# Kernel optimization log

Measured on AMD Instinct MI355X. Metric: run time of the kernel, lower is better.

## Reference

```python
import jax, jax.numpy as jnp
import numpy as np

B, C, H, W = 2, 256, 64, 64
NUM_HEADS = 4
DIM_HEAD_QK = 64
DIM_HEAD_V = 64  # dim_out // num_heads
DIM_OUT_QK = NUM_HEADS * DIM_HEAD_QK  # 256
DIM_OUT_V = NUM_HEADS * DIM_HEAD_V    # 256
SCALE = DIM_HEAD_QK ** -0.5


def rel_logits_1d(q, rel_k, permute):
    # q: (Bh, Hq, Wq, d), rel_k: (2*Wq-1, d)
    Bh, Hq, Wq, d = q.shape
    R = 2 * Wq - 1
    x = jnp.einsum('bhwd,rd->bhwr', q, rel_k)              # (Bh, Hq, Wq, R)
    x = x.reshape(-1, Wq, R)
    x_pad = jnp.pad(x, ((0, 0), (0, 0), (0, 1))).reshape(x.shape[0], -1)
    x_pad = jnp.pad(x_pad, ((0, 0), (0, Wq - 1)))
    x_pad = x_pad.reshape(-1, Wq + 1, R)
    x = x_pad[:, :Wq, Wq - 1:]                              # (Bh*Hq, Wq, Wq)
    x = x.reshape(Bh, Hq, 1, Wq, Wq)
    x = jnp.broadcast_to(x, (Bh, Hq, Hq, Wq, Wq))
    return jnp.transpose(x, permute)


def pos_embed_rel(q, height_rel, width_rel):
    # q: (Bh, HW, d)
    Bh = q.shape[0]
    qr = q.reshape(Bh, H, W, -1)
    rel_w = rel_logits_1d(qr, width_rel, (0, 1, 3, 2, 4))   # (Bh, H, W, H, W)
    qt = jnp.transpose(qr, (0, 2, 1, 3))                    # (Bh, W, H, d)
    rel_h = rel_logits_1d(qt, height_rel, (0, 3, 1, 4, 2))  # (Bh, H, W, H, W)
    return (rel_h + rel_w).reshape(Bh, H * W, H * W)


def setup_inputs() -> dict:
    key = jax.random.key(0)
    k1, k2, k3, k4 = jax.random.split(key, 4)
    x = jax.random.normal(k1, (B, C, H, W), dtype=jnp.float32)
    qkv_w = jax.random.normal(k2, (2 * DIM_OUT_QK + DIM_OUT_V, C), dtype=jnp.float32) * (C ** -0.5)
    height_rel = jax.random.normal(k3, (2 * H - 1, DIM_HEAD_QK), dtype=jnp.float32) * SCALE
    width_rel = jax.random.normal(k4, (2 * W - 1, DIM_HEAD_QK), dtype=jnp.float32) * SCALE
    return {"x": x, "qkv_w": qkv_w, "height_rel": height_rel, "width_rel": width_rel}


def reference(x, qkv_w, height_rel, width_rel):
    # 1x1 conv == channel matmul
    qkv = jnp.einsum('bchw,oc->bohw', x, qkv_w)             # (B, 768, H, W)
    q, k, v = jnp.split(qkv, [DIM_OUT_QK, 2 * DIM_OUT_QK], axis=1)
    HW = H * W
    q = q.reshape(B * NUM_HEADS, DIM_HEAD_QK, HW).transpose(0, 2, 1)  # (Bh, HW, d)
    k = k.reshape(B * NUM_HEADS, DIM_HEAD_QK, HW)                     # (Bh, d, HW)
    v = v.reshape(B * NUM_HEADS, DIM_HEAD_V, HW).transpose(0, 2, 1)   # (Bh, HW, dv)
    attn = jnp.einsum('bnd,bdm->bnm', q, k) * SCALE + pos_embed_rel(q, height_rel, width_rel)
    attn = jax.nn.softmax(attn, axis=-1)
    out = jnp.einsum('bnm,bmd->bnd', attn, v)               # (Bh, HW, dv)
    out = out.transpose(0, 2, 1).reshape(B, DIM_OUT_V, H, W)
    return out
```

## Files before the change

kernel.cpp:

```cpp
#include <hip/hip_runtime.h>
#include <hip/hip_bf16.h>

typedef __attribute__((ext_vector_type(8))) short bf16x8;
typedef __attribute__((ext_vector_type(4))) float f32x4;

static __device__ __forceinline__ f32x4 mfma16(bf16x8 a, bf16x8 b, f32x4 c) {
    return __builtin_amdgcn_mfma_f32_16x16x32_bf16(a, b, c, 0, 0, 0);
}
static __device__ __forceinline__ void gll16(const void* g, void* l) {
    __builtin_amdgcn_global_load_lds(
        (const __attribute__((address_space(1))) unsigned int*)g,
        (__attribute__((address_space(3))) unsigned int*)l, 16, 0, 0);
}

#define LOG2E 1.44269504f

__global__ __launch_bounds__(256, 4) void qkv_kernel(
    const float* __restrict__ x, const float* __restrict__ w,
    __hip_bfloat16* __restrict__ qb, __hip_bfloat16* __restrict__ kb,
    __hip_bfloat16* __restrict__ vt)
{
    alignas(16) __shared__ __hip_bfloat16 sA[64 * 72];
    alignas(16) __shared__ __hip_bfloat16 sB[64 * 72];
    const int nb = blockIdx.x * 64;
    const int ob = blockIdx.y * 64;
    const int b  = blockIdx.z;
    const int tid  = threadIdx.x;
    const int lane = tid & 63;
    const int wv   = tid >> 6;
    const int quad = lane >> 4;
    const int l16  = lane & 15;

    f32x4 acc[4];
    for (int i = 0; i < 4; i++) acc[i] = (f32x4)0.f;

    const int oA = tid >> 2, cA = (tid & 3) << 4;
    const float* srcw = w + (ob + oA) * 256 + cA;
    const int cB = tid >> 2, nB = (tid & 3) << 4;
    const int csw = cB ^ ((tid & 3) * 16);
    const float* srcx = x + ((size_t)b * 256 + cB) * 4096 + nb + nB;

    float4 ra[4], rb4[4];
    #pragma unroll
    for (int i = 0; i < 4; i++) ra[i]  = *(const float4*)(srcw + i * 4);
    #pragma unroll
    for (int i = 0; i < 4; i++) rb4[i] = *(const float4*)(srcx + i * 4);

    for (int t = 0; t < 4; t++) {
        __syncthreads();
        {
            union { bf16x8 v; __hip_bfloat16 h[8]; } u0, u1;
            #pragma unroll
            for (int i = 0; i < 2; i++) {
                float4 f = ra[i];
                u0.h[4*i+0] = __float2bfloat16(f.x); u0.h[4*i+1] = __float2bfloat16(f.y);
                u0.h[4*i+2] = __float2bfloat16(f.z); u0.h[4*i+3] = __float2bfloat16(f.w);
            }
            #pragma unroll
            for (int i = 0; i < 2; i++) {
                float4 f = ra[2 + i];
                u1.h[4*i+0] = __float2bfloat16(f.x); u1.h[4*i+1] = __float2bfloat16(f.y);
                u1.h[4*i+2] = __float2bfloat16(f.z); u1.h[4*i+3] = __float2bfloat16(f.w);
            }
            *(bf16x8*)&sA[oA * 72 + cA]     = u0.v;
            *(bf16x8*)&sA[oA * 72 + cA + 8] = u1.v;
        }
        {
            #pragma unroll
            for (int i = 0; i < 4; i++) {
                float4 f = rb4[i];
                sB[(nB + 4*i + 0) * 72 + csw] = __float2bfloat16(f.x);
                sB[(nB + 4*i + 1) * 72 + csw] = __float2bfloat16(f.y);
                sB[(nB + 4*i + 2) * 72 + csw] = __float2bfloat16(f.z);
                sB[(nB + 4*i + 3) * 72 + csw] = __float2bfloat16(f.w);
            }
        }
        __syncthreads();
        if (t < 3) {
            #pragma unroll
            for (int i = 0; i < 4; i++)
                ra[i]  = *(const float4*)(srcw + (t + 1) * 64 + i * 4);
            #pragma unroll
            for (int i = 0; i < 4; i++)
                rb4[i] = *(const float4*)(srcx + (size_t)(t + 1) * 64 * 4096 + i * 4);
        }
        const __hip_bfloat16* aRow = &sA[(16 * wv + l16) * 72];
        #pragma unroll
        for (int ks = 0; ks < 2; ks++) {
            bf16x8 af = *(const bf16x8*)&aRow[ks * 32 + quad * 8];
            #pragma unroll
            for (int ct = 0; ct < 4; ct++) {
                bf16x8 bfv = *(const bf16x8*)&sB[(16 * ct + l16) * 72
                                                 + ((ks * 32 + quad * 8) ^ (ct * 16))];
                acc[ct] = mfma16(af, bfv, acc[ct]);
            }
        }
    }
    if (ob < 512) {
        __syncthreads();
        #pragma unroll
        for (int ct = 0; ct < 4; ct++) {
            union { short4 s; __hip_bfloat16 hh[4]; } u;
            #pragma unroll
            for (int r = 0; r < 4; r++) u.hh[r] = __float2bfloat16(acc[ct][r]);
            *(short4*)&sA[(16 * ct + l16) * 72 + 16 * wv + 4 * quad] = u.s;
        }
        __syncthreads();
        const int n_l = tid >> 2, d16 = (tid & 3) * 16;
        const int n = nb + n_l;
        const __hip_bfloat16* srcl = &sA[n_l * 72 + d16];
        bf16x8 v0 = *(const bf16x8*)srcl;
        bf16x8 v1 = *(const bf16x8*)(srcl + 8);
        const int bhh = b * 4 + ((ob & 255) >> 6);
        if (ob < 256) {
            __hip_bfloat16* dst = qb + ((size_t)bhh * 4096 + n) * 64;
            *(bf16x8*)(dst + d16)     = v0;
            *(bf16x8*)(dst + d16 + 8) = v1;
        } else {
            const int s = (n & 7) << 3;
            __hip_bfloat16* dst = kb + ((size_t)bhh * 4096 + n) * 64;
            *(bf16x8*)(dst + (d16 ^ s))       = v0;
            *(bf16x8*)(dst + ((d16 + 8) ^ s)) = v1;
        }
    } else {
        __syncthreads();
        #pragma unroll
        for (int ct = 0; ct < 4; ct++)
            #pragma unroll
            for (int r = 0; r < 4; r++)
                sA[(16 * wv + quad * 4 + r) * 72 + 16 * ct + l16] = __float2bfloat16(acc[ct][r]);
        int o2 = (ob - 512) + 16 * wv + l16;
        int bhh = b * 4 + (o2 >> 6), d = o2 & 63;
        const __hip_bfloat16* srcl = &sA[(16 * wv + l16) * 72 + 16 * quad];
        __hip_bfloat16* vrow = vt + ((size_t)bhh * 64 + d) * 4096;
        const int kt = quad & 1;
        const int gbase = nb + (quad >> 1) * 32;
        const int dsw = (d & 7) << 3;
        #pragma unroll
        for (int m = 0; m < 4; m++) {
            short4 val = *(const short4*)(srcl + 4 * m);
            int P4 = gbase + 8 * m + 4 * kt;
            *(short4*)(vrow + (P4 ^ dsw)) = val;
        }
    }
}

__global__ __launch_bounds__(512, 4) void attn_kernel(
    const __hip_bfloat16* __restrict__ qb, const __hip_bfloat16* __restrict__ kb,
    const __hip_bfloat16* __restrict__ vt, const float* __restrict__ hrel,
    const float* __restrict__ wrel, float* __restrict__ out)
{
    extern __shared__ __align__(16) char smem[];
    alignas(16) __shared__ __hip_bfloat16 sRH[64 * 66];

    const int h    = blockIdx.x;
    const int bh   = blockIdx.y;
    const int tid  = threadIdx.x;
    const int lane = tid & 63;
    const int wv   = tid >> 6;
    const int qg   = wv >> 2;
    const int kg   = wv & 3;
    const int quad = lane >> 4;
    const int l16  = lane & 15;

    __hip_bfloat16* sQ   = (__hip_bfloat16*)smem;
    __hip_bfloat16* sW   = (__hip_bfloat16*)smem + 64 * 72;
    __hip_bfloat16* sHRs = (__hip_bfloat16*)smem + 192 * 72;
    __hip_bfloat16* sRWt = (__hip_bfloat16*)smem;

    {
        int r = tid >> 3, d8 = (tid & 7) * 8;
        *(bf16x8*)&sQ[r * 72 + d8] =
            *(const bf16x8*)&qb[(((size_t)bh * 4096 + h * 64 + r)) * 64 + d8];
    }
    {
        int r = tid >> 2, c0 = (tid & 3) << 4;
        union { bf16x8 v; __hip_bfloat16 h8[8]; } u0, u1;
        #pragma unroll
        for (int i = 0; i < 2; i++) {
            float4 f = (r < 127) ? *(const float4*)&wrel[r * 64 + c0 + 4*i] : float4{0,0,0,0};
            u0.h8[4*i+0] = __float2bfloat16(f.x); u0.h8[4*i+1] = __float2bfloat16(f.y);
            u0.h8[4*i+2] = __float2bfloat16(f.z); u0.h8[4*i+3] = __float2bfloat16(f.w);
        }
        #pragma unroll
        for (int i = 0; i < 2; i++) {
            float4 f = (r < 127) ? *(const float4*)&wrel[r * 64 + c0 + 8 + 4*i] : float4{0,0,0,0};
            u1.h8[4*i+0] = __float2bfloat16(f.x); u1.h8[4*i+1] = __float2bfloat16(f.y);
            u1.h8[4*i+2] = __float2bfloat16(f.z); u1.h8[4*i+3] = __float2bfloat16(f.w);
        }
        *(bf16x8*)&sW[r * 72 + c0]     = u0.v;
        *(bf16x8*)&sW[r * 72 + c0 + 8] = u1.v;
    }
    {
        int r = tid >> 3, c0 = (tid & 7) * 8;
        union { bf16x8 v; __hip_bfloat16 h8[8]; } u0;
        #pragma unroll
        for (int i = 0; i < 2; i++) {
            float4 f = *(const float4*)&hrel[(63 - h + r) * 64 + c0 + 4*i];
            u0.h8[4*i+0] = __float2bfloat16(f.x); u0.h8[4*i+1] = __float2bfloat16(f.y);
            u0.h8[4*i+2] = __float2bfloat16(f.z); u0.h8[4*i+3] = __float2bfloat16(f.w);
        }
        *(bf16x8*)&sHRs[r * 72 + c0] = u0.v;
    }
    __syncthreads();

    const int g    = wv & 3;
    const int half = wv >> 2;
    const __hip_bfloat16* aRow = &sQ[(16 * g + l16) * 72];
    bf16x8 qf0 = *(const bf16x8*)&aRow[quad * 8];
    bf16x8 qf1 = *(const bf16x8*)&aRow[32 + quad * 8];
    bf16x8 qm[2][2];
    #pragma unroll
    for (int qt = 0; qt < 2; qt++) {
        const __hip_bfloat16* qr = &sQ[(qg * 32 + 16 * qt + l16) * 72];
        qm[qt][0] = *(const bf16x8*)&qr[quad * 8];
        qm[qt][1] = *(const bf16x8*)&qr[32 + quad * 8];
    }
    __syncthreads();

    {
        const int rbase = half * 64;
        #pragma unroll
        for (int ct = 0; ct < 4; ct++) {
            int rr = rbase + 16 * ct + l16;
            f32x4 a = (f32x4)0.f;
            a = mfma16(qf0, *(const bf16x8*)&sW[rr * 72 + quad * 8], a);
            a = mfma16(qf1, *(const bf16x8*)&sW[rr * 72 + 32 + quad * 8], a);
            #pragma unroll
            for (int r = 0; r < 4; r++) {
                int ww = 16 * g + quad * 4 + r;
                int wp = rr + ww - 63;
                if (wp >= 0 && wp < 64) sRWt[ww * 68 + wp] = __float2bfloat16(a[r]);
            }
        }
    }
    if (half == 0) {
        #pragma unroll
        for (int ct = 0; ct < 4; ct++) {
            f32x4 a = (f32x4)0.f;
            a = mfma16(qf0, *(const bf16x8*)&sHRs[(16 * ct + l16) * 72 + quad * 8], a);
            a = mfma16(qf1, *(const bf16x8*)&sHRs[(16 * ct + l16) * 72 + 32 + quad * 8], a);
            #pragma unroll
            for (int r = 0; r < 4; r++)
                sRH[(16 * g + quad * 4 + r) * 66 + 16 * ct + l16] = __float2bfloat16(a[r]);
        }
    }
    __syncthreads();

    union S4 { short4 s; __hip_bfloat16 h[4]; };
    float rwf[2][2][4];
    #pragma unroll
    for (int qt = 0; qt < 2; qt++)
        #pragma unroll
        for (int kt = 0; kt < 2; kt++) {
            S4 t;
            t.s = *(const short4*)&sRWt[(qg * 32 + 16 * qt + l16) * 68
                                        + 32 * (kg & 1) + 16 * kt + 4 * quad];
            #pragma unroll
            for (int r = 0; r < 4; r++)
                rwf[qt][kt][r] = LOG2E * __bfloat162float(t.h[r]);
        }
    __syncthreads();

    const char* kT = (const char*)kb + (size_t)bh * 524288 + wv * 1024 + lane * 16;
    const char* vT = (const char*)vt + (size_t)bh * 524288
                     + (size_t)(wv * 4 + quad) * 8192 + l16 * 16;

    gll16(kT,                smem + wv * 1024);
    gll16(kT + 8192,         smem + 8192 + wv * 1024);
    gll16(vT,                smem + 16384 + wv * 1024);
    gll16(vT + 262144,       smem + 24576 + wv * 1024);
    gll16(kT + 16384,        smem + 32768 + wv * 1024);
    gll16(kT + 16384 + 8192, smem + 32768 + 8192 + wv * 1024);
    gll16(vT + 256,          smem + 32768 + 16384 + wv * 1024);
    gll16(vT + 262144 + 256, smem + 32768 + 24576 + wv * 1024);

    f32x4 oacc[2][4];
    #pragma unroll
    for (int qt = 0; qt < 2; qt++)
        #pragma unroll
        for (int dt = 0; dt < 4; dt++) oacc[qt][dt] = (f32x4)0.f;
    f32x4 lacc[2] = {(f32x4)0.f, (f32x4)0.f};
    const bf16x8 vones = (bf16x8)(short)0x3F80;

    const int krowOff = (kg * 32 + l16) * 128;
    const int sw  = (l16 & 7) << 4;
    const int kA  = (quad * 16) ^ sw;
    const int kB  = (64 + quad * 16) ^ sw;
    const int vOff = 16384 + l16 * 256 + ((kg * 64 + quad * 16) ^ sw);

    const __hip_bfloat16* rh0 = &sRH[(qg * 32 + l16) * 66];
    const __hip_bfloat16* rh1 = &sRH[(qg * 32 + 16 + l16) * 66];
    const float SC = 0.125f * LOG2E;

    for (int j = 0; j < 32; j++) {
        const char* buf = smem + (j & 1) * 32768;
        if (j < 31) asm volatile("s_waitcnt vmcnt(4)" ::: "memory");
        else        asm volatile("s_waitcnt vmcnt(0)" ::: "memory");
        __builtin_amdgcn_s_barrier();
        __builtin_amdgcn_sched_barrier(0);

        const char* kr = buf + krowOff;
        bf16x8 kf00 = *(const bf16x8*)(kr + kA);
        bf16x8 kf01 = *(const bf16x8*)(kr + kB);
        bf16x8 kf10 = *(const bf16x8*)(kr + 2048 + kA);
        bf16x8 kf11 = *(const bf16x8*)(kr + 2048 + kB);

        f32x4 s[2][2];
        __builtin_amdgcn_s_setprio(1);
        #pragma unroll
        for (int qt = 0; qt < 2; qt++) {
            f32x4 a0 = (f32x4)0.f, a1 = (f32x4)0.f;
            a0 = mfma16(kf00, qm[qt][0], a0);
            a0 = mfma16(kf01, qm[qt][1], a0);
            a1 = mfma16(kf10, qm[qt][0], a1);
            a1 = mfma16(kf11, qm[qt][1], a1);
            s[qt][0] = a0; s[qt][1] = a1;
        }
        __builtin_amdgcn_s_setprio(0);

        const int hp = 2 * j + (kg >> 1);
        bf16x8 pa[2];
        #pragma unroll
        for (int qt = 0; qt < 2; qt++) {
            float rhb = LOG2E * __bfloat162float((qt ? rh1 : rh0)[hp]);
            float pv[8];
            #pragma unroll
            for (int r = 0; r < 4; r++)
                pv[r] = __builtin_amdgcn_exp2f(fmaf(s[qt][0][r], SC, rwf[qt][0][r] + rhb));
            #pragma unroll
            for (int r = 0; r < 4; r++)
                pv[4 + r] = __builtin_amdgcn_exp2f(fmaf(s[qt][1][r], SC, rwf[qt][1][r] + rhb));
            union { bf16x8 v; __hip_bfloat162 b2[4]; } pu;
            #pragma unroll
            for (int pi = 0; pi < 4; pi++)
                pu.b2[pi] = __float22bfloat162_rn(float2{pv[2 * pi], pv[2 * pi + 1]});
            pa[qt] = pu.v;
        }

        __builtin_amdgcn_s_setprio(1);
        #pragma unroll
        for (int dt = 0; dt < 4; dt++) {
            bf16x8 vf = *(const bf16x8*)(buf + vOff + dt * 4096);
            oacc[0][dt] = mfma16(pa[0], vf, oacc[0][dt]);
            oacc[1][dt] = mfma16(pa[1], vf, oacc[1][dt]);
        }
        lacc[0] = mfma16(pa[0], vones, lacc[0]);
        lacc[1] = mfma16(pa[1], vones, lacc[1]);
        __builtin_amdgcn_s_setprio(0);

        __builtin_amdgcn_sched_barrier(0);
        __builtin_amdgcn_s_barrier();
        if (j < 30) {
            char* nb2 = smem + (j & 1) * 32768;
            const char* gk = kT + (size_t)(j + 2) * 16384;
            gll16(gk,          nb2 + wv * 1024);
            gll16(gk + 8192,   nb2 + 8192 + wv * 1024);
            const char* gv = vT + (size_t)(j + 2) * 256;
            gll16(gv,          nb2 + 16384 + wv * 1024);
            gll16(gv + 262144, nb2 + 24576 + wv * 1024);
        }
    }

    float* obuf = (float*)smem;
    if (kg != 0) {
        float* rb = obuf + (kg - 1) * 4672;
        #pragma unroll
        for (int qt = 0; qt < 2; qt++)
            #pragma unroll
            for (int dt = 0; dt < 4; dt++)
                *(f32x4*)&rb[qg * 2304 + (16 * dt + l16) * 36 + 16 * qt + 4 * quad]
                    = oacc[qt][dt];
        if (l16 == 0)
            #pragma unroll
            for (int qt = 0; qt < 2; qt++)
                #pragma unroll
                for (int r = 0; r < 4; r++)
                    rb[4608 + qg * 32 + 16 * qt + 4 * quad + r] = lacc[qt][r];
    }
    __syncthreads();
    if (kg == 0) {
        #pragma unroll
        for (int rg = 0; rg < 3; rg++) {
            const float* rb = obuf + rg * 4672;
            #pragma unroll
            for (int qt = 0; qt < 2; qt++) {
                #pragma unroll
                for (int dt = 0; dt < 4; dt++)
                    oacc[qt][dt] += *(const f32x4*)&rb[qg * 2304 + (16 * dt + l16) * 36
                                                       + 16 * qt + 4 * quad];
                #pragma unroll
                for (int r = 0; r < 4; r++)
                    lacc[qt][r] += rb[4608 + qg * 32 + 16 * qt + 4 * quad + r];
            }
        }
        const int b = bh >> 2, head = bh & 3;
        #pragma unroll
        for (int qt = 0; qt < 2; qt++) {
            f32x4 lv;
            #pragma unroll
            for (int r = 0; r < 4; r++) lv[r] = 1.f / lacc[qt][r];
            #pragma unroll
            for (int dt = 0; dt < 4; dt++) {
                f32x4 o = oacc[qt][dt] * lv;
                int dv = 16 * dt + l16;
                int q0 = qg * 32 + 16 * qt + 4 * quad;
                *(f32x4*)&out[((size_t)(b * 256 + head * 64 + dv)) * 4096 + h * 64 + q0] = o;
            }
        }
    }
}

extern "C" void kernel_launch(void* const* d_in, const int* in_sizes, int n_in,
                              void* d_out, int out_size, void* d_ws, size_t ws_size,
                              hipStream_t stream) {
    const float* x     = (const float*)d_in[0];
    const float* qkv_w = (const float*)d_in[1];
    const float* hrel  = (const float*)d_in[2];
    const float* wrel  = (const float*)d_in[3];
    float* out = (float*)d_out;

    __hip_bfloat16* qb = (__hip_bfloat16*)d_ws;
    __hip_bfloat16* kb = qb + (size_t)8 * 4096 * 64;
    __hip_bfloat16* vt = kb + (size_t)8 * 4096 * 64;

    qkv_kernel<<<dim3(64, 12, 2), 256, 0, stream>>>(x, qkv_w, qb, kb, vt);
    attn_kernel<<<dim3(64, 8), 512, 65536, stream>>>(qb, kb, vt, hrel, wrel, out);
}
```

Baseline: 127.8 us.

## Replace LDS double-buffered K/V staging with direct global register loads

Drops the global_load_lds double-buffering of K and V tiles through shared memory, along with the per-iteration barriers and vmcnt waits. Each wave now loads its K and V fragments straight from global memory (L2) into registers, prefetching the next K tile one step ahead with a ping-pong register pair. The rel-width bias is kept as packed bf16 and converted inside the loop instead of being held as floats. This removes LDS traffic and block-wide synchronisation, but adds redundant global loads across waves, exposes V-load latency within each step, and raises register pressure.

```diff
diff --git a/kernel.cpp b/kernel.cpp
--- a/kernel.cpp
+++ b/kernel.cpp
@@ -6,11 +6,6 @@
 
 static __device__ __forceinline__ f32x4 mfma16(bf16x8 a, bf16x8 b, f32x4 c) {
     return __builtin_amdgcn_mfma_f32_16x16x32_bf16(a, b, c, 0, 0, 0);
-}
-static __device__ __forceinline__ void gll16(const void* g, void* l) {
-    __builtin_amdgcn_global_load_lds(
-        (const __attribute__((address_space(1))) unsigned int*)g,
-        (__attribute__((address_space(3))) unsigned int*)l, 16, 0, 0);
 }
 
 #define LOG2E 1.44269504f
@@ -248,32 +243,14 @@
     __syncthreads();
 
     union S4 { short4 s; __hip_bfloat16 h[4]; };
-    float rwf[2][2][4];
+    S4 rwp[2][2];
     #pragma unroll
     for (int qt = 0; qt < 2; qt++)
         #pragma unroll
-        for (int kt = 0; kt < 2; kt++) {
-            S4 t;
-            t.s = *(const short4*)&sRWt[(qg * 32 + 16 * qt + l16) * 68
-                                        + 32 * (kg & 1) + 16 * kt + 4 * quad];
-            #pragma unroll
-            for (int r = 0; r < 4; r++)
-                rwf[qt][kt][r] = LOG2E * __bfloat162float(t.h[r]);
-        }
+        for (int kt = 0; kt < 2; kt++)
+            rwp[qt][kt].s = *(const short4*)&sRWt[(qg * 32 + 16 * qt + l16) * 68
+                                                  + 32 * (kg & 1) + 16 * kt + 4 * quad];
     __syncthreads();
-
-    const char* kT = (const char*)kb + (size_t)bh * 524288 + wv * 1024 + lane * 16;
-    const char* vT = (const char*)vt + (size_t)bh * 524288
-                     + (size_t)(wv * 4 + quad) * 8192 + l16 * 16;
-
-    gll16(kT,                smem + wv * 1024);
-    gll16(kT + 8192,         smem + 8192 + wv * 1024);
-    gll16(vT,                smem + 16384 + wv * 1024);
-    gll16(vT + 262144,       smem + 24576 + wv * 1024);
-    gll16(kT + 16384,        smem + 32768 + wv * 1024);
-    gll16(kT + 16384 + 8192, smem + 32768 + 8192 + wv * 1024);
-    gll16(vT + 256,          smem + 32768 + 16384 + wv * 1024);
-    gll16(vT + 262144 + 256, smem + 32768 + 24576 + wv * 1024);
 
     f32x4 oacc[2][4];
     #pragma unroll
@@ -283,84 +260,101 @@
     f32x4 lacc[2] = {(f32x4)0.f, (f32x4)0.f};
     const bf16x8 vones = (bf16x8)(short)0x3F80;
 
-    const int krowOff = (kg * 32 + l16) * 128;
     const int sw  = (l16 & 7) << 4;
-    const int kA  = (quad * 16) ^ sw;
-    const int kB  = (64 + quad * 16) ^ sw;
-    const int vOff = 16384 + l16 * 256 + ((kg * 64 + quad * 16) ^ sw);
+    const int ko0 = (quad * 16) ^ sw;
+    const int ko1 = (64 + quad * 16) ^ sw;
+    const char* kgb = (const char*)kb + (size_t)bh * 524288 + (kg * 32 + l16) * 128;
+    const char* vgb = (const char*)vt + (size_t)bh * 524288 + (size_t)l16 * 8192
+                      + ((kg * 64 + quad * 16) ^ sw);
 
     const __hip_bfloat16* rh0 = &sRH[(qg * 32 + l16) * 66];
     const __hip_bfloat16* rh1 = &sRH[(qg * 32 + 16 + l16) * 66];
     const float SC = 0.125f * LOG2E;
 
-    for (int j = 0; j < 32; j++) {
-        const char* buf = smem + (j & 1) * 32768;
-        if (j < 31) asm volatile("s_waitcnt vmcnt(4)" ::: "memory");
-        else        asm volatile("s_waitcnt vmcnt(0)" ::: "memory");
-        __builtin_amdgcn_s_barrier();
-        __builtin_amdgcn_sched_barrier(0);
-
-        const char* kr = buf + krowOff;
-        bf16x8 kf00 = *(const bf16x8*)(kr + kA);
-        bf16x8 kf01 = *(const bf16x8*)(kr + kB);
-        bf16x8 kf10 = *(const bf16x8*)(kr + 2048 + kA);
-        bf16x8 kf11 = *(const bf16x8*)(kr + 2048 + kB);
-
-        f32x4 s[2][2];
-        __builtin_amdgcn_s_setprio(1);
-        #pragma unroll
-        for (int qt = 0; qt < 2; qt++) {
-            f32x4 a0 = (f32x4)0.f, a1 = (f32x4)0.f;
-            a0 = mfma16(kf00, qm[qt][0], a0);
-            a0 = mfma16(kf01, qm[qt][1], a0);
-            a1 = mfma16(kf10, qm[qt][0], a1);
-            a1 = mfma16(kf11, qm[qt][1], a1);
-            s[qt][0] = a0; s[qt][1] = a1;
-        }
-        __builtin_amdgcn_s_setprio(0);
-
-        const int hp = 2 * j + (kg >> 1);
-        bf16x8 pa[2];
-        #pragma unroll
-        for (int qt = 0; qt < 2; qt++) {
-            float rhb = LOG2E * __bfloat162float((qt ? rh1 : rh0)[hp]);
-            float pv[8];
-            #pragma unroll
-            for (int r = 0; r < 4; r++)
-                pv[r] = __builtin_amdgcn_exp2f(fmaf(s[qt][0][r], SC, rwf[qt][0][r] + rhb));
-            #pragma unroll
-            for (int r = 0; r < 4; r++)
-                pv[4 + r] = __builtin_amdgcn_exp2f(fmaf(s[qt][1][r], SC, rwf[qt][1][r] + rhb));
-            union { bf16x8 v; __hip_bfloat162 b2[4]; } pu;
-            #pragma unroll
-            for (int pi = 0; pi < 4; pi++)
-                pu.b2[pi] = __float22bfloat162_rn(float2{pv[2 * pi], pv[2 * pi + 1]});
-            pa[qt] = pu.v;
-        }
-
-        __builtin_amdgcn_s_setprio(1);
-        #pragma unroll
-        for (int dt = 0; dt < 4; dt++) {
-            bf16x8 vf = *(const bf16x8*)(buf + vOff + dt * 4096);
-            oacc[0][dt] = mfma16(pa[0], vf, oacc[0][dt]);
-            oacc[1][dt] = mfma16(pa[1], vf, oacc[1][dt]);
-        }
-        lacc[0] = mfma16(pa[0], vones, lacc[0]);
-        lacc[1] = mfma16(pa[1], vones, lacc[1]);
-        __builtin_amdgcn_s_setprio(0);
-
-        __builtin_amdgcn_sched_barrier(0);
-        __builtin_amdgcn_s_barrier();
-        if (j < 30) {
-            char* nb2 = smem + (j & 1) * 32768;
-            const char* gk = kT + (size_t)(j + 2) * 16384;
-            gll16(gk,          nb2 + wv * 1024);
-            gll16(gk + 8192,   nb2 + 8192 + wv * 1024);
-            const char* gv = vT + (size_t)(j + 2) * 256;
-            gll16(gv,          nb2 + 16384 + wv * 1024);
-            gll16(gv + 262144, nb2 + 24576 + wv * 1024);
-        }
-    }
+#define LOAD_K(D, jj) do {                                        \
+        const char* kp_ = kgb + (size_t)(jj) * 16384;             \
+        D##0 = *(const bf16x8*)(kp_ + ko0);                       \
+        D##1 = *(const bf16x8*)(kp_ + ko1);                       \
+        D##2 = *(const bf16x8*)(kp_ + 2048 + ko0);                \
+        D##3 = *(const bf16x8*)(kp_ + 2048 + ko1);                \
+    } while (0)
+
+#define STEP(jj, KC, KN, doPref) do {                                          \
+        const char* vp_ = vgb + (size_t)(jj) * 256;                            \
+        bf16x8 vv0 = *(const bf16x8*)(vp_);                                    \
+        bf16x8 vv1 = *(const bf16x8*)(vp_ + 131072);                           \
+        bf16x8 vv2 = *(const bf16x8*)(vp_ + 262144);                           \
+        bf16x8 vv3 = *(const bf16x8*)(vp_ + 393216);                           \
+        if (doPref) LOAD_K(KN, (jj) + 1);                                      \
+        f32x4 s00, s01, s10, s11;                                              \
+        __builtin_amdgcn_s_setprio(1);                                         \
+        s00 = mfma16(KC##0, qm[0][0], (f32x4)0.f);                             \
+        s00 = mfma16(KC##1, qm[0][1], s00);                                    \
+        s10 = mfma16(KC##2, qm[0][0], (f32x4)0.f);                             \
+        s10 = mfma16(KC##3, qm[0][1], s10);                                    \
+        s01 = mfma16(KC##0, qm[1][0], (f32x4)0.f);                             \
+        s01 = mfma16(KC##1, qm[1][1], s01);                                    \
+        s11 = mfma16(KC##2, qm[1][0], (f32x4)0.f);                             \
+        s11 = mfma16(KC##3, qm[1][1], s11);                                    \
+        __builtin_amdgcn_s_setprio(0);                                         \
+        const int hp_ = 2 * (jj) + (kg >> 1);                                  \
+        float rhb0 = LOG2E * __bfloat162float(rh0[hp_]);                       \
+        float rhb1 = LOG2E * __bfloat162float(rh1[hp_]);                       \
+        bf16x8 pa0, pa1;                                                       \
+        {                                                                      \
+            float pvv[8];                                                      \
+            _Pragma("unroll")                                                  \
+            for (int r = 0; r < 4; r++)                                        \
+                pvv[r] = __builtin_amdgcn_exp2f(fmaf(s00[r], SC,               \
+                    fmaf(__bfloat162float(rwp[0][0].h[r]), LOG2E, rhb0)));     \
+            _Pragma("unroll")                                                  \
+            for (int r = 0; r < 4; r++)                                        \
+                pvv[4 + r] = __builtin_amdgcn_exp2f(fmaf(s10[r], SC,           \
+                    fmaf(__bfloat162float(rwp[0][1].h[r]), LOG2E, rhb0)));     \
+            union { bf16x8 v; __hip_bfloat162 b2[4]; } pu;                     \
+            _Pragma("unroll")                                                  \
+            for (int pi = 0; pi < 4; pi++)                                     \
+                pu.b2[pi] = __float22bfloat162_rn(float2{pvv[2*pi], pvv[2*pi+1]}); \
+            pa0 = pu.v;                                                        \
+        }                                                                      \
+        {                                                                      \
+            float pvv[8];                                                      \
+            _Pragma("unroll")                                                  \
+            for (int r = 0; r < 4; r++)                                        \
+                pvv[r] = __builtin_amdgcn_exp2f(fmaf(s01[r], SC,               \
+                    fmaf(__bfloat162float(rwp[1][0].h[r]), LOG2E, rhb1)));     \
+            _Pragma("unroll")                                                  \
+            for (int r = 0; r < 4; r++)                                        \
+                pvv[4 + r] = __builtin_amdgcn_exp2f(fmaf(s11[r], SC,           \
+                    fmaf(__bfloat162float(rwp[1][1].h[r]), LOG2E, rhb1)));     \
+            union { bf16x8 v; __hip_bfloat162 b2[4]; } pu;                     \
+            _Pragma("unroll")                                                  \
+            for (int pi = 0; pi < 4; pi++)                                     \
+                pu.b2[pi] = __float22bfloat162_rn(float2{pvv[2*pi], pvv[2*pi+1]}); \
+            pa1 = pu.v;                                                        \
+        }                                                                      \
+        __builtin_amdgcn_s_setprio(1);                                         \
+        oacc[0][0] = mfma16(pa0, vv0, oacc[0][0]);                             \
+        oacc[1][0] = mfma16(pa1, vv0, oacc[1][0]);                             \
+        oacc[0][1] = mfma16(pa0, vv1, oacc[0][1]);                             \
+        oacc[1][1] = mfma16(pa1, vv1, oacc[1][1]);                             \
+        oacc[0][2] = mfma16(pa0, vv2, oacc[0][2]);                             \
+        oacc[1][2] = mfma16(pa1, vv2, oacc[1][2]);                             \
+        oacc[0][3] = mfma16(pa0, vv3, oacc[0][3]);                             \
+        oacc[1][3] = mfma16(pa1, vv3, oacc[1][3]);                             \
+        lacc[0] = mfma16(pa0, vones, lacc[0]);                                 \
+        lacc[1] = mfma16(pa1, vones, lacc[1]);                                 \
+        __builtin_amdgcn_s_setprio(0);                                         \
+    } while (0)
+
+    bf16x8 ka0, ka1, ka2, ka3, kn0, kn1, kn2, kn3;
+    LOAD_K(ka, 0);
+    for (int j = 0; j < 32; j += 2) {
+        STEP(j,     ka, kn, 1);
+        STEP(j + 1, kn, ka, (j + 1 < 31));
+    }
+#undef STEP
+#undef LOAD_K
 
     float* obuf = (float*)smem;
     if (kg != 0) {
```

New measurement: 383.8 us. +200.5%, slower.
